# Kernel tuning notes

Hardware: AMD Instinct MI355X
Metric: run time of the kernel (lower is better)

## Reference

```python
import jax, jax.numpy as jnp
import numpy as np

N, E, D, H, G, C = 50000, 800000, 128, 128, 256, 10
BN_EPS = 1e-5

def _lin_init(key, fan_in, fan_out):
    k1, k2 = jax.random.split(key)
    bound = 1.0 / np.sqrt(fan_in)
    w = jax.random.uniform(k1, (fan_in, fan_out), jnp.float32, -bound, bound)
    b = jax.random.uniform(k2, (fan_out,), jnp.float32, -bound, bound)
    return w, b

def setup_inputs() -> dict:
    key = jax.random.key(0)
    ks = jax.random.split(key, 16)
    x = jax.random.normal(ks[0], (N, D), jnp.float32)
    edge_index = jax.random.randint(ks[1], (2, E), 0, N, jnp.int64)
    batch = jnp.sort(jax.random.randint(ks[2], (N,), 0, G, jnp.int64))
    inp = {"x": x, "edge_index": edge_index, "batch": batch}
    # per-layer GIN MLP params: Linear-ReLU-Linear-ReLU-BN
    dims = [(D, H), (H, H), (H, H)]
    for i, (din, dh) in enumerate(dims, start=1):
        wa, ba = _lin_init(ks[2 + 2 * i], din, dh)
        wb, bb = _lin_init(ks[3 + 2 * i], dh, dh)
        inp[f"w{i}a"], inp[f"b{i}a"] = wa, ba
        inp[f"w{i}b"], inp[f"b{i}b"] = wb, bb
        inp[f"g{i}"] = jnp.ones((dh,), jnp.float32)
        inp[f"bt{i}"] = jnp.zeros((dh,), jnp.float32)
    inp["eps"] = jnp.zeros((3,), jnp.float32)  # train_eps=True, init 0
    inp["lw1"], inp["lb1"] = _lin_init(ks[10], H, H)
    inp["lw2"], inp["lb2"] = _lin_init(ks[11], H, C)
    return inp

def _gin_layer(x, src, dst, eps_i, wa, ba, wb, bb, g, bt):
    # scatter-add neighbor aggregation: out[i] = sum_{j->i} x[j]
    agg = jax.ops.segment_sum(x[src], dst, num_segments=N)
    h = (1.0 + eps_i) * x + agg
    h = jax.nn.relu(h @ wa + ba)
    h = jax.nn.relu(h @ wb + bb)
    mu = h.mean(axis=0)
    var = ((h - mu) ** 2).mean(axis=0)  # biased var (torch BN normalization)
    return g * (h - mu) * jax.lax.rsqrt(var + BN_EPS) + bt

def reference(x, edge_index, batch, w1a, b1a, w1b, b1b, g1, bt1,
              w2a, b2a, w2b, b2b, g2, bt2, w3a, b3a, w3b, b3b, g3, bt3,
              eps, lw1, lb1, lw2, lb2):
    src, dst = edge_index[0], edge_index[1]
    h = _gin_layer(x, src, dst, eps[0], w1a, b1a, w1b, b1b, g1, bt1)
    h = _gin_layer(h, src, dst, eps[1], w2a, b2a, w2b, b2b, g2, bt2)
    h = _gin_layer(h, src, dst, eps[2], w3a, b3a, w3b, b3b, g3, bt3)
    # global mean pool over batch ids
    sums = jax.ops.segment_sum(h, batch, num_segments=G)
    cnt = jax.ops.segment_sum(jnp.ones((N,), h.dtype), batch, num_segments=G)
    pooled = sums / jnp.maximum(cnt, 1.0)[:, None]
    z = jax.nn.relu(pooled @ lw1 + lb1)
    # dropout omitted (eval / deterministic reference)
    z = z @ lw2 + lb2
    return jax.nn.log_softmax(z, axis=-1)
```

## Files before the change

kernel.cpp:

```cpp
#include <hip/hip_runtime.h>

#define N_NODES 50000
#define N_EDGES 800000
#define DIM 128
#define N_GRAPHS 256
#define N_CLS 10
#define BN_EPSV 1e-5f
#define CAP 64
#define RSIZE 6250
#define NBLK ((N_NODES + 63) / 64)

typedef __attribute__((ext_vector_type(8))) short short8;
typedef __attribute__((ext_vector_type(4))) float f32x4;

__device__ __forceinline__ float bf2f(short u) {
  return __uint_as_float(((unsigned)(unsigned short)u) << 16);
}
__device__ __forceinline__ unsigned short f2bf(float f) {
  unsigned u = __float_as_uint(f);
  unsigned r = (u + 0x7FFFu + ((u >> 16) & 1u)) >> 16;
  return (unsigned short)r;
}
__device__ __forceinline__ int swz(int row, int bytecol) {
  return row * 256 + (bytecol ^ ((row & 7) << 4));
}


__global__ void cvt_x_kernel(const float* __restrict__ x, ushort* __restrict__ xb) {
  int i = blockIdx.x * blockDim.x + threadIdx.x;
  int stride = gridDim.x * blockDim.x;
  const int tot = N_NODES * DIM / 4;
  for (; i < tot; i += stride) {
    float4 v = ((const float4*)x)[i];
    ushort4 o;
    o.x = f2bf(v.x); o.y = f2bf(v.y); o.z = f2bf(v.z); o.w = f2bf(v.w);
    ((ushort4*)xb)[i] = o;
  }
}

__global__ void cvt_w_kernel(const float* __restrict__ w0, const float* __restrict__ w1,
                             const float* __restrict__ w2, const float* __restrict__ w3,
                             const float* __restrict__ w4, const float* __restrict__ w5,
                             ushort* __restrict__ wt) {
  int m = blockIdx.x >> 6;
  const float* w = m == 0 ? w0 : m == 1 ? w1 : m == 2 ? w2 : m == 3 ? w3
                                                       : m == 4 ? w4 : w5;
  int idx = (blockIdx.x & 63) * 256 + threadIdx.x;
  int k = idx >> 7, n = idx & 127;
  wt[m * 16384 + n * 128 + k] = f2bf(w[idx]);
}


__global__ __launch_bounds__(256) void fill_kernel(
    const int* __restrict__ src, const int* __restrict__ dst,
    int* __restrict__ cnt, ushort* __restrict__ csr) {
  int cls = blockIdx.x & 7;
  int lo = cls * RSIZE;
  int hi = lo + RSIZE;
  int i = (blockIdx.x >> 3) * blockDim.x + threadIdx.x;
  int stride = (gridDim.x >> 3) * blockDim.x;
  for (; i < N_EDGES; i += stride) {
    int d = dst[i];
    if (d >= lo && d < hi) {
      int p = atomicAdd(&cnt[d], 1);
      if (p < CAP) csr[(size_t)d * CAP + p] = (ushort)src[i];
    }
  }
}


template <bool FIRST>
__global__ __launch_bounds__(512, 8) void layer_kernel(
    const ushort* __restrict__ xin, const int* __restrict__ cnt,
    const ushort* __restrict__ csr, const float* __restrict__ pstats,
    const float* __restrict__ pgamma, const float* __restrict__ pbeta,
    const float* __restrict__ epsp, int layer,
    const ushort* __restrict__ W1T, const float* __restrict__ b1,
    const ushort* __restrict__ W2T, const float* __restrict__ b2,
    ushort* __restrict__ out, float* __restrict__ bstat) {
  __shared__ __align__(16) ushort As[64 * DIM];
  __shared__ __align__(16) ushort H1[64 * DIM];
  __shared__ float sums[8 * DIM];
  __shared__ float sqs[8 * DIM];
  int tid = threadIdx.x;
  int w8 = tid >> 6;
  int l = tid & 63, li = l & 15, lg = l >> 4;
  int row0 = blockIdx.x * 64;
  float epv = 1.0f + epsp[layer];
  float sc8[8], sh8[8];
  if (!FIRST) {
    const float invN = 1.0f / N_NODES;
#pragma unroll
    for (int j = 0; j < 8; j++) {
      int c = li * 8 + j;
      float mu = pstats[c] * invN;
      float var = fmaxf(pstats[DIM + c] * invN - mu * mu, 0.f);
      float sc = pgamma[c] * rsqrtf(var + BN_EPSV);
      sc8[j] = sc;
      sh8[j] = pbeta[c] - mu * sc;
    }
  }
  for (int n = 0; n < 8; n++) {
    int nl = w8 * 8 + n;
    int node = row0 + nl;
    float av[8];
#pragma unroll
    for (int j = 0; j < 8; j++) av[j] = 0.f;
    if (node < N_NODES) {
      int deg = cnt[node];
      deg = deg < CAP ? deg : CAP;
      const ushort* nb = csr + (size_t)node * CAP;
      if (lg == 0) {
        short8 sv = *(const short8*)(xin + (size_t)node * DIM + li * 8);
#pragma unroll
        for (int j = 0; j < 8; j++) av[j] = epv * bf2f(sv[j]);
      }
      int i = lg;
      for (; i + 12 < deg; i += 16) {
        int j0 = nb[i], j1 = nb[i + 4], j2 = nb[i + 8], j3 = nb[i + 12];
        short8 v0 = *(const short8*)(xin + (size_t)j0 * DIM + li * 8);
        short8 v1 = *(const short8*)(xin + (size_t)j1 * DIM + li * 8);
        short8 v2 = *(const short8*)(xin + (size_t)j2 * DIM + li * 8);
        short8 v3 = *(const short8*)(xin + (size_t)j3 * DIM + li * 8);
#pragma unroll
        for (int j = 0; j < 8; j++)
          av[j] += (bf2f(v0[j]) + bf2f(v1[j])) + (bf2f(v2[j]) + bf2f(v3[j]));
      }
      for (; i < deg; i += 4) {
        int j0 = nb[i];
        short8 v0 = *(const short8*)(xin + (size_t)j0 * DIM + li * 8);
#pragma unroll
        for (int j = 0; j < 8; j++) av[j] += bf2f(v0[j]);
      }
#pragma unroll
      for (int j = 0; j < 8; j++) {
        av[j] += __shfl_xor(av[j], 16, 64);
        av[j] += __shfl_xor(av[j], 32, 64);
      }
      if (!FIRST && lg == 0) {
        float co = epv + (float)deg;
#pragma unroll
        for (int j = 0; j < 8; j++) av[j] = sc8[j] * av[j] + co * sh8[j];
      }
    }
    if (lg == 0) {
      short8 uv;
#pragma unroll
      for (int j = 0; j < 8; j++) uv[j] = (short)f2bf(av[j]);
      *(short8*)((char*)As + swz(nl, li * 16)) = uv;
    }
  }
  __syncthreads();
  int wg = w8 >> 1;
  int ch = w8 & 1;
  {
    f32x4 acc[4] = {};
    short8 af[4];
#pragma unroll
    for (int ks = 0; ks < 4; ks++)
      af[ks] = *(const short8*)((char*)As + swz(16 * wg + li, ks * 64 + lg * 16));
#pragma unroll
    for (int ct4 = 0; ct4 < 4; ct4++) {
      int ct = ch * 4 + ct4;
      const char* wp = (const char*)W1T + (ct * 16 + li) * 256 + lg * 16;
#pragma unroll
      for (int ks = 0; ks < 4; ks++) {
        short8 bf = *(const short8*)(wp + ks * 64);
        acc[ct4] = __builtin_amdgcn_mfma_f32_16x16x32_bf16(af[ks], bf, acc[ct4], 0, 0, 0);
      }
    }
#pragma unroll
    for (int ct4 = 0; ct4 < 4; ct4++) {
      int ct = ch * 4 + ct4;
      float bv = b1[ct * 16 + li];
#pragma unroll
      for (int r = 0; r < 4; r++) {
        int row = 16 * wg + lg * 4 + r;
        *(ushort*)((char*)H1 + swz(row, (ct * 16 + li) * 2)) =
            f2bf(fmaxf(acc[ct4][r] + bv, 0.f));
      }
    }
  }
  __syncthreads();
  float ss[4] = {0, 0, 0, 0}, sq[4] = {0, 0, 0, 0};
  {
    f32x4 acc[4] = {};
    short8 af[4];
#pragma unroll
    for (int ks = 0; ks < 4; ks++)
      af[ks] = *(const short8*)((char*)H1 + swz(16 * wg + li, ks * 64 + lg * 16));
#pragma unroll
    for (int ct4 = 0; ct4 < 4; ct4++) {
      int ct = ch * 4 + ct4;
      const char* wp = (const char*)W2T + (ct * 16 + li) * 256 + lg * 16;
#pragma unroll
      for (int ks = 0; ks < 4; ks++) {
        short8 bf = *(const short8*)(wp + ks * 64);
        acc[ct4] = __builtin_amdgcn_mfma_f32_16x16x32_bf16(af[ks], bf, acc[ct4], 0, 0, 0);
      }
    }
#pragma unroll
    for (int ct4 = 0; ct4 < 4; ct4++) {
      int ct = ch * 4 + ct4;
      float bv = b2[ct * 16 + li];
#pragma unroll
      for (int r = 0; r < 4; r++) {
        int row = 16 * wg + lg * 4 + r;
        float v = fmaxf(acc[ct4][r] + bv, 0.f);
        *(ushort*)((char*)As + swz(row, (ct * 16 + li) * 2)) = f2bf(v);
        float vm = (row0 + row < N_NODES) ? v : 0.f;
        ss[ct4] += vm;
        sq[ct4] += vm * vm;
      }
    }
  }
#pragma unroll
  for (int ct4 = 0; ct4 < 4; ct4++) {
    ss[ct4] += __shfl_xor(ss[ct4], 16, 64);
    ss[ct4] += __shfl_xor(ss[ct4], 32, 64);
    sq[ct4] += __shfl_xor(sq[ct4], 16, 64);
    sq[ct4] += __shfl_xor(sq[ct4], 32, 64);
  }
  if (l < 16) {
#pragma unroll
    for (int ct4 = 0; ct4 < 4; ct4++) {
      sums[w8 * DIM + (ch * 4 + ct4) * 16 + l] = ss[ct4];
      sqs[w8 * DIM + (ch * 4 + ct4) * 16 + l] = sq[ct4];
      sums[w8 * DIM + ((1 - ch) * 4 + ct4) * 16 + l] = 0.f;
      sqs[w8 * DIM + ((1 - ch) * 4 + ct4) * 16 + l] = 0.f;
    }
  }
  __syncthreads();
  for (int t = tid; t < 1024; t += 512) {
    int row = t >> 4, chunk = t & 15;
    int grow = row0 + row;
    if (grow < N_NODES) {
      short8 v = *(const short8*)((char*)As + swz(row, chunk * 16));
      *(short8*)(out + (size_t)grow * DIM + chunk * 8) = v;
    }
  }
  if (tid < DIM) {
    float t1 = 0.f, t2 = 0.f;
#pragma unroll
    for (int g = 0; g < 8; g++) {
      t1 += sums[g * DIM + tid];
      t2 += sqs[g * DIM + tid];
    }
    bstat[(size_t)blockIdx.x * DIM + tid] = t1;
    bstat[((size_t)NBLK + blockIdx.x) * DIM + tid] = t2;
  }
}


__global__ __launch_bounds__(64) void stats_reduce_kernel(
    const float* __restrict__ bstat, float* __restrict__ stats) {
  int c = blockIdx.x;
  int t = threadIdx.x;
  const float* src = bstat + (c < DIM ? 0 : (size_t)NBLK * DIM) + (c & (DIM - 1));
  float a = 0.f;
  for (int b = t; b < NBLK; b += 64) a += src[(size_t)b * DIM];
#pragma unroll
  for (int m = 32; m >= 1; m >>= 1) a += __shfl_xor(a, m, 64);
  if (t == 0) stats[c] = a;
}


__global__ void bounds_kernel(const int* __restrict__ batch, int* __restrict__ gstart) {
  int i = blockIdx.x * blockDim.x + threadIdx.x;
  if (i >= N_NODES) return;
  int b = batch[i];
  int prev = (i == 0) ? -1 : batch[i - 1];
  for (int g = prev + 1; g <= b; g++) gstart[g] = i;
  if (i == N_NODES - 1)
    for (int g = b + 1; g <= N_GRAPHS; g++) gstart[g] = N_NODES;
}


__global__ __launch_bounds__(128) void pool2_kernel(const ushort* __restrict__ h,
    const int* __restrict__ gstart, float* __restrict__ pool) {
  int g = blockIdx.x, t = threadIdx.x;
  int s = gstart[g], e = gstart[g + 1];
  float a0 = 0.f, a1 = 0.f, a2 = 0.f, a3 = 0.f;
  int i = s;
  for (; i + 3 < e; i += 4) {
    a0 += bf2f((short)h[(size_t)(i + 0) * DIM + t]);
    a1 += bf2f((short)h[(size_t)(i + 1) * DIM + t]);
    a2 += bf2f((short)h[(size_t)(i + 2) * DIM + t]);
    a3 += bf2f((short)h[(size_t)(i + 3) * DIM + t]);
  }
  for (; i < e; i++) a0 += bf2f((short)h[(size_t)i * DIM + t]);
  float cn = (float)(e - s);
  if (cn < 1.f) cn = 1.f;
  pool[g * DIM + t] = ((a0 + a1) + (a2 + a3)) / cn;
}


__global__ __launch_bounds__(128) void final_kernel(const float* __restrict__ pool,
    const float* __restrict__ stats3,
    const float* __restrict__ gamma3, const float* __restrict__ beta3,
    const float* __restrict__ lw1, const float* __restrict__ lb1,
    const float* __restrict__ lw2, const float* __restrict__ lb2,
    float* __restrict__ out) {
  int g = blockIdx.x, t = threadIdx.x;
  __shared__ float p[DIM];
  __shared__ float part[2];
  __shared__ float z2[N_CLS];
  const float invN = 1.0f / N_NODES;
  float mu = stats3[t] * invN;
  float var = fmaxf(stats3[DIM + t] * invN - mu * mu, 0.f);
  float sc = gamma3[t] * rsqrtf(var + BN_EPSV);
  float sh = beta3[t] - mu * sc;
  p[t] = sc * pool[g * DIM + t] + sh;
  __syncthreads();
  float acc = lb1[t];
  for (int k = 0; k < DIM; k++) acc += p[k] * lw1[k * DIM + t];
  acc = fmaxf(acc, 0.f);
  for (int c = 0; c < N_CLS; c++) {
    float v = acc * lw2[t * N_CLS + c];
#pragma unroll
    for (int m = 32; m >= 1; m >>= 1) v += __shfl_xor(v, m, 64);
    if ((t & 63) == 0) part[t >> 6] = v;
    __syncthreads();
    if (t == 0) z2[c] = part[0] + part[1] + lb2[c];
    __syncthreads();
  }
  if (t == 0) {
    float mx = -1e30f;
    for (int c = 0; c < N_CLS; c++) mx = fmaxf(mx, z2[c]);
    float sum = 0.f;
    for (int c = 0; c < N_CLS; c++) sum += expf(z2[c] - mx);
    float lse = mx + logf(sum);
    for (int c = 0; c < N_CLS; c++) out[g * N_CLS + c] = z2[c] - lse;
  }
}


extern "C" void kernel_launch(void* const* d_in, const int* in_sizes, int n_in,
                              void* d_out, int out_size, void* d_ws, size_t ws_size,
                              hipStream_t stream) {
  const float* x = (const float*)d_in[0];
  const int* edge = (const int*)d_in[1];
  const int* batch = (const int*)d_in[2];
  const float *w[3][2], *bv[3][2], *gam[3], *bet[3];
  int idx = 3;
  for (int l = 0; l < 3; l++) {
    w[l][0] = (const float*)d_in[idx++]; bv[l][0] = (const float*)d_in[idx++];
    w[l][1] = (const float*)d_in[idx++]; bv[l][1] = (const float*)d_in[idx++];
    gam[l] = (const float*)d_in[idx++];  bet[l] = (const float*)d_in[idx++];
  }
  const float* eps = (const float*)d_in[idx++];
  const float* lw1 = (const float*)d_in[idx++];
  const float* lb1 = (const float*)d_in[idx++];
  const float* lw2 = (const float*)d_in[idx++];
  const float* lb2 = (const float*)d_in[idx++];

  char* ws = (char*)d_ws;
  size_t off_b = 0;
  auto alloc = [&](size_t b) -> char* {
    char* p = ws + off_b;
    off_b += (b + 255) & ~(size_t)255;
    return p;
  };
  int* cnt = (int*)alloc((size_t)N_NODES * 4);
  ushort* csr = (ushort*)alloc((size_t)N_NODES * CAP * 2);
  ushort* P0 = (ushort*)alloc((size_t)N_NODES * DIM * 2);
  ushort* P1 = (ushort*)alloc((size_t)N_NODES * DIM * 2);
  ushort* wt = (ushort*)alloc((size_t)6 * 16384 * 2);
  float* stats = (float*)alloc(3 * 2 * DIM * 4);
  float* pool = (float*)alloc((size_t)N_GRAPHS * DIM * 4);
  int* gstart = (int*)alloc((size_t)(N_GRAPHS + 1) * 4);
  float* bstat = (float*)alloc((size_t)2 * NBLK * DIM * 4);

  hipMemsetAsync(cnt, 0, (size_t)N_NODES * 4, stream);

  const int* srcp = edge;
  const int* dstp = edge + N_EDGES;
  cvt_x_kernel<<<2048, 256, 0, stream>>>(x, P0);
  cvt_w_kernel<<<384, 256, 0, stream>>>(w[0][0], w[0][1], w[1][0], w[1][1],
                                        w[2][0], w[2][1], wt);
  fill_kernel<<<2048, 256, 0, stream>>>(srcp, dstp, cnt, csr);
  bounds_kernel<<<(N_NODES + 255) / 256, 256, 0, stream>>>(batch, gstart);

  layer_kernel<true><<<NBLK, 512, 0, stream>>>(
      P0, cnt, csr, nullptr, nullptr, nullptr, eps, 0,
      wt + 0 * 16384, bv[0][0], wt + 1 * 16384, bv[0][1], P1, bstat);
  stats_reduce_kernel<<<256, 64, 0, stream>>>(bstat, stats);
  layer_kernel<false><<<NBLK, 512, 0, stream>>>(
      P1, cnt, csr, stats, gam[0], bet[0], eps, 1,
      wt + 2 * 16384, bv[1][0], wt + 3 * 16384, bv[1][1], P0, bstat);
  stats_reduce_kernel<<<256, 64, 0, stream>>>(bstat, stats + 2 * DIM);
  layer_kernel<false><<<NBLK, 512, 0, stream>>>(
      P0, cnt, csr, stats + 2 * DIM, gam[1], bet[1], eps, 2,
      wt + 4 * 16384, bv[2][0], wt + 5 * 16384, bv[2][1], P1, bstat);
  stats_reduce_kernel<<<256, 64, 0, stream>>>(bstat, stats + 4 * DIM);

  pool2_kernel<<<N_GRAPHS, 128, 0, stream>>>(P1, gstart, pool);
  final_kernel<<<N_GRAPHS, 128, 0, stream>>>(pool, stats + 4 * DIM,
                                             gam[2], bet[2], lw1, lb1, lw2, lb2,
                                             (float*)d_out);
}
```

Baseline: 314.6 us.

## Merge prep kernels into one launch and pad neighbor gather with zero row

```diff
diff --git a/kernel.cpp b/kernel.cpp
--- a/kernel.cpp
+++ b/kernel.cpp
@@ -9,6 +9,7 @@
 #define CAP 64
 #define RSIZE 6250
 #define NBLK ((N_NODES + 63) / 64)
+#define ZROW N_NODES
 
 typedef __attribute__((ext_vector_type(8))) short short8;
 typedef __attribute__((ext_vector_type(4))) float f32x4;
@@ -26,28 +27,47 @@
 }
 
 
-__global__ void cvt_x_kernel(const float* __restrict__ x, ushort* __restrict__ xb) {
-  int i = blockIdx.x * blockDim.x + threadIdx.x;
-  int stride = gridDim.x * blockDim.x;
-  const int tot = N_NODES * DIM / 4;
-  for (; i < tot; i += stride) {
-    float4 v = ((const float4*)x)[i];
-    ushort4 o;
-    o.x = f2bf(v.x); o.y = f2bf(v.y); o.z = f2bf(v.z); o.w = f2bf(v.w);
-    ((ushort4*)xb)[i] = o;
-  }
-}
-
-__global__ void cvt_w_kernel(const float* __restrict__ w0, const float* __restrict__ w1,
-                             const float* __restrict__ w2, const float* __restrict__ w3,
-                             const float* __restrict__ w4, const float* __restrict__ w5,
-                             ushort* __restrict__ wt) {
-  int m = blockIdx.x >> 6;
-  const float* w = m == 0 ? w0 : m == 1 ? w1 : m == 2 ? w2 : m == 3 ? w3
-                                                       : m == 4 ? w4 : w5;
-  int idx = (blockIdx.x & 63) * 256 + threadIdx.x;
-  int k = idx >> 7, n = idx & 127;
-  wt[m * 16384 + n * 128 + k] = f2bf(w[idx]);
+__global__ __launch_bounds__(256) void prep_kernel(
+    const float* __restrict__ x, ushort* __restrict__ xb,
+    const float* __restrict__ w0, const float* __restrict__ w1,
+    const float* __restrict__ w2, const float* __restrict__ w3,
+    const float* __restrict__ w4, const float* __restrict__ w5,
+    ushort* __restrict__ wt, const int* __restrict__ batch,
+    int* __restrict__ gstart, int* __restrict__ cnt,
+    ushort* __restrict__ z0, ushort* __restrict__ z1) {
+  int bid = blockIdx.x, tid = threadIdx.x;
+  if (bid < 384) {
+    int m = bid >> 6;
+    const float* w = m == 0 ? w0 : m == 1 ? w1 : m == 2 ? w2 : m == 3 ? w3
+                                                         : m == 4 ? w4 : w5;
+    int idx = (bid & 63) * 256 + tid;
+    int k = idx >> 7, n = idx & 127;
+    wt[m * 16384 + n * 128 + k] = f2bf(w[idx]);
+  } else if (bid < 384 + 2048) {
+    const int tot = N_NODES * DIM / 4;
+    int i = (bid - 384) * 256 + tid;
+    for (; i < tot; i += 2048 * 256) {
+      float4 v = ((const float4*)x)[i];
+      ushort4 o;
+      o.x = f2bf(v.x); o.y = f2bf(v.y); o.z = f2bf(v.z); o.w = f2bf(v.w);
+      ((ushort4*)xb)[i] = o;
+    }
+  } else if (bid < 384 + 2048 + 196) {
+    int i = (bid - (384 + 2048)) * 256 + tid;
+    if (i < N_NODES) {
+      cnt[i] = 0;
+      int b = batch[i];
+      int prev = (i == 0) ? -1 : batch[i - 1];
+      for (int g = prev + 1; g <= b; g++) gstart[g] = i;
+      if (i == N_NODES - 1)
+        for (int g = b + 1; g <= N_GRAPHS; g++) gstart[g] = N_NODES;
+    }
+  } else {
+    if (tid < DIM) {
+      z0[(size_t)ZROW * DIM + tid] = 0;
+      z1[(size_t)ZROW * DIM + tid] = 0;
+    }
+  }
 }
 
 
@@ -87,18 +107,16 @@
   int l = tid & 63, li = l & 15, lg = l >> 4;
   int row0 = blockIdx.x * 64;
   float epv = 1.0f + epsp[layer];
-  float sc8[8], sh8[8];
   if (!FIRST) {
-    const float invN = 1.0f / N_NODES;
-#pragma unroll
-    for (int j = 0; j < 8; j++) {
-      int c = li * 8 + j;
-      float mu = pstats[c] * invN;
-      float var = fmaxf(pstats[DIM + c] * invN - mu * mu, 0.f);
-      float sc = pgamma[c] * rsqrtf(var + BN_EPSV);
-      sc8[j] = sc;
-      sh8[j] = pbeta[c] - mu * sc;
-    }
+    if (tid < DIM) {
+      const float invN = 1.0f / N_NODES;
+      float mu = pstats[tid] * invN;
+      float var = fmaxf(pstats[DIM + tid] * invN - mu * mu, 0.f);
+      float sc = pgamma[tid] * rsqrtf(var + BN_EPSV);
+      sums[tid] = sc;
+      sqs[tid] = pbeta[tid] - mu * sc;
+    }
+    __syncthreads();
   }
   for (int n = 0; n < 8; n++) {
     int nl = w8 * 8 + n;
@@ -115,9 +133,17 @@
 #pragma unroll
         for (int j = 0; j < 8; j++) av[j] = epv * bf2f(sv[j]);
       }
-      int i = lg;
-      for (; i + 12 < deg; i += 16) {
-        int j0 = nb[i], j1 = nb[i + 4], j2 = nb[i + 8], j3 = nb[i + 12];
+      int nbat = (deg + 15) >> 4;
+      for (int b = 0; b < nbat; b++) {
+        int i0 = b * 16 + lg, i1 = i0 + 4, i2 = i0 + 8, i3 = i0 + 12;
+        int r0 = nb[i0 < deg ? i0 : 0];
+        int r1 = nb[i1 < deg ? i1 : 0];
+        int r2 = nb[i2 < deg ? i2 : 0];
+        int r3 = nb[i3 < deg ? i3 : 0];
+        int j0 = i0 < deg ? r0 : ZROW;
+        int j1 = i1 < deg ? r1 : ZROW;
+        int j2 = i2 < deg ? r2 : ZROW;
+        int j3 = i3 < deg ? r3 : ZROW;
         short8 v0 = *(const short8*)(xin + (size_t)j0 * DIM + li * 8);
         short8 v1 = *(const short8*)(xin + (size_t)j1 * DIM + li * 8);
         short8 v2 = *(const short8*)(xin + (size_t)j2 * DIM + li * 8);
@@ -126,12 +152,6 @@
         for (int j = 0; j < 8; j++)
           av[j] += (bf2f(v0[j]) + bf2f(v1[j])) + (bf2f(v2[j]) + bf2f(v3[j]));
       }
-      for (; i < deg; i += 4) {
-        int j0 = nb[i];
-        short8 v0 = *(const short8*)(xin + (size_t)j0 * DIM + li * 8);
-#pragma unroll
-        for (int j = 0; j < 8; j++) av[j] += bf2f(v0[j]);
-      }
 #pragma unroll
       for (int j = 0; j < 8; j++) {
         av[j] += __shfl_xor(av[j], 16, 64);
@@ -140,7 +160,8 @@
       if (!FIRST && lg == 0) {
         float co = epv + (float)deg;
 #pragma unroll
-        for (int j = 0; j < 8; j++) av[j] = sc8[j] * av[j] + co * sh8[j];
+        for (int j = 0; j < 8; j++)
+          av[j] = sums[li * 8 + j] * av[j] + co * sqs[li * 8 + j];
       }
     }
     if (lg == 0) {
@@ -262,17 +283,6 @@
 #pragma unroll
   for (int m = 32; m >= 1; m >>= 1) a += __shfl_xor(a, m, 64);
   if (t == 0) stats[c] = a;
-}
-
-
-__global__ void bounds_kernel(const int* __restrict__ batch, int* __restrict__ gstart) {
-  int i = blockIdx.x * blockDim.x + threadIdx.x;
-  if (i >= N_NODES) return;
-  int b = batch[i];
-  int prev = (i == 0) ? -1 : batch[i - 1];
-  for (int g = prev + 1; g <= b; g++) gstart[g] = i;
-  if (i == N_NODES - 1)
-    for (int g = b + 1; g <= N_GRAPHS; g++) gstart[g] = N_NODES;
 }
 
 
@@ -363,23 +373,20 @@
   };
   int* cnt = (int*)alloc((size_t)N_NODES * 4);
   ushort* csr = (ushort*)alloc((size_t)N_NODES * CAP * 2);
-  ushort* P0 = (ushort*)alloc((size_t)N_NODES * DIM * 2);
-  ushort* P1 = (ushort*)alloc((size_t)N_NODES * DIM * 2);
+  ushort* P0 = (ushort*)alloc((size_t)(N_NODES + 1) * DIM * 2);
+  ushort* P1 = (ushort*)alloc((size_t)(N_NODES + 1) * DIM * 2);
   ushort* wt = (ushort*)alloc((size_t)6 * 16384 * 2);
   float* stats = (float*)alloc(3 * 2 * DIM * 4);
   float* pool = (float*)alloc((size_t)N_GRAPHS * DIM * 4);
   int* gstart = (int*)alloc((size_t)(N_GRAPHS + 1) * 4);
   float* bstat = (float*)alloc((size_t)2 * NBLK * DIM * 4);
 
-  hipMemsetAsync(cnt, 0, (size_t)N_NODES * 4, stream);
-
   const int* srcp = edge;
   const int* dstp = edge + N_EDGES;
-  cvt_x_kernel<<<2048, 256, 0, stream>>>(x, P0);
-  cvt_w_kernel<<<384, 256, 0, stream>>>(w[0][0], w[0][1], w[1][0], w[1][1],
-                                        w[2][0], w[2][1], wt);
+  prep_kernel<<<384 + 2048 + 196 + 1, 256, 0, stream>>>(
+      x, P0, w[0][0], w[0][1], w[1][0], w[1][1], w[2][0], w[2][1], wt,
+      batch, gstart, cnt, P0, P1);
   fill_kernel<<<2048, 256, 0, stream>>>(srcp, dstp, cnt, csr);
-  bounds_kernel<<<(N_NODES + 255) / 256, 256, 0, stream>>>(batch, gstart);
 
   layer_kernel<true><<<NBLK, 512, 0, stream>>>(
       P0, cnt, csr, nullptr, nullptr, nullptr, eps, 0,
```

New measurement: 278.0 us. 1.13x faster.
